# Kernel optimization log

Measured on AMD Instinct MI355X. Metric: run time of the kernel, lower is better.

The kernel has to match this reference:

```python
import jax, jax.numpy as jnp
import numpy as np

D = 128          # fine voxel grid resolution
N0 = 250000
D_IN, D_BASE, D_OUT = 16, 8, 8
EPS = 1e-5
# (cin, cout) for conv0..conv6, conv7, conv9, conv11
_CH = [(16, 8), (8, 16), (16, 16), (16, 32), (32, 32), (32, 64), (64, 64), (64, 32), (32, 16), (16, 8)]

def _offsets():
    r = np.arange(-1, 2)
    return np.stack(np.meshgrid(r, r, r, indexing='ij'), -1).reshape(-1, 3)  # [27,3]

def _lookup_fn(coords, d):
    keys = (coords[:, 0].astype(np.int64) * d + coords[:, 1]) * d + coords[:, 2]
    order = np.argsort(keys)
    skeys = keys[order]
    def lookup(q):
        valid = ((q >= 0) & (q < d)).all(-1)
        k = (q[:, 0].astype(np.int64) * d + q[:, 1]) * d + q[:, 2]
        pos = np.clip(np.searchsorted(skeys, k), 0, len(skeys) - 1)
        return np.where(valid & (skeys[pos] == k), order[pos], -1).astype(np.int32)
    return lookup

def _nbr_same(coords, d):
    # stride-1 sparse conv: outputs at input coords, neighbors at coord+k
    lk = _lookup_fn(coords, d)
    return np.stack([lk(coords + o) for o in _offsets()], 1)  # [N,27]

def _nbr_down(c_out, c_in, d_in):
    # stride-2 conv: output p gathers inputs at 2p+k
    lk = _lookup_fn(c_in, d_in)
    return np.stack([lk(c_out * 2 + o) for o in _offsets()], 1)

def _nbr_up(c_out, c_in, d_in):
    # transposed stride-2 conv: output q gathers input p=(q-k)/2 where divisible
    lk = _lookup_fn(c_in, d_in)
    cols = []
    for o in _offsets():
        q = c_out - o
        div = (q % 2 == 0).all(-1)
        cols.append(np.where(div, lk(q // 2), -1).astype(np.int32))
    return np.stack(cols, 1)

def setup_inputs():
    rng = np.random.default_rng(0)
    flat = rng.choice(D ** 3, size=N0, replace=False)
    c0 = np.stack([flat // (D * D), (flat // D) % D, flat % D], 1).astype(np.int32)
    c1 = np.unique(c0 // 2, axis=0)
    c2 = np.unique(c1 // 2, axis=0)
    c3 = np.unique(c2 // 2, axis=0)
    inp = {
        'feats': jax.random.normal(jax.random.key(0), (N0, D_IN), jnp.float32),
        'nbr0': jnp.asarray(_nbr_same(c0, D)),
        'nbr_d01': jnp.asarray(_nbr_down(c1, c0, D)),
        'nbr1': jnp.asarray(_nbr_same(c1, D // 2)),
        'nbr_d12': jnp.asarray(_nbr_down(c2, c1, D // 2)),
        'nbr2': jnp.asarray(_nbr_same(c2, D // 4)),
        'nbr_d23': jnp.asarray(_nbr_down(c3, c2, D // 4)),
        'nbr3': jnp.asarray(_nbr_same(c3, D // 8)),
        'nbr_u32': jnp.asarray(_nbr_up(c2, c3, D // 8)),
        'nbr_u21': jnp.asarray(_nbr_up(c1, c2, D // 4)),
        'nbr_u10': jnp.asarray(_nbr_up(c0, c1, D // 2)),
    }
    key = jax.random.key(1)
    for i, (ci, co) in enumerate(_CH):
        key, kw = jax.random.split(key)
        inp['w%d' % i] = jax.random.normal(kw, (27, ci, co), jnp.float32) / np.sqrt(27.0 * ci)
        inp['g%d' % i] = jnp.ones((co,), jnp.float32)
        inp['b%d' % i] = jnp.zeros((co,), jnp.float32)
    inp['lin_w'] = jax.random.normal(jax.random.key(2), (D_OUT, D_BASE), jnp.float32) / np.sqrt(D_BASE)
    return inp

def _sconv_bn_relu(f, nbr, w, g, b):
    # f: [Nin,Cin], nbr: [Nout,27] (-1 = no neighbor), w: [27,Cin,Cout]
    gth = jnp.where((nbr >= 0)[..., None], f[jnp.maximum(nbr, 0)], 0.0)  # [Nout,27,Cin]
    y = jnp.einsum('nkc,kco->no', gth, w)
    mu = y.mean(0)                       # training-mode BatchNorm over active voxels
    var = y.var(0)
    return jax.nn.relu((y - mu) * jax.lax.rsqrt(var + EPS) * g + b)

def reference(feats, nbr0, nbr_d01, nbr1, nbr_d12, nbr2, nbr_d23, nbr3, nbr_u32, nbr_u21, nbr_u10,
              w0, g0, b0, w1, g1, b1, w2, g2, b2, w3, g3, b3, w4, g4, b4,
              w5, g5, b5, w6, g6, b6, w7, g7, b7, w8, g8, b8, w9, g9, b9, lin_w):
    c0f = _sconv_bn_relu(feats, nbr0, w0, g0, b0)
    c2f = _sconv_bn_relu(_sconv_bn_relu(c0f, nbr_d01, w1, g1, b1), nbr1, w2, g2, b2)
    c4f = _sconv_bn_relu(_sconv_bn_relu(c2f, nbr_d12, w3, g3, b3), nbr2, w4, g4, b4)
    x = _sconv_bn_relu(_sconv_bn_relu(c4f, nbr_d23, w5, g5, b5), nbr3, w6, g6, b6)
    x = c4f + _sconv_bn_relu(x, nbr_u32, w7, g7, b7)
    x = c2f + _sconv_bn_relu(x, nbr_u21, w8, g8, b8)
    x = c0f + _sconv_bn_relu(x, nbr_u10, w9, g9, b9)
    return x @ lin_w.T, x
```

## Files before the change

kernel.cpp:

```cpp
#include <hip/hip_runtime.h>

#define EPSV 1e-5f
#define NBUCKET 64

typedef __attribute__((ext_vector_type(8))) short short8;
typedef __attribute__((ext_vector_type(4))) float float4v;

static inline int cdiv(int a, int b) { return (a + b - 1) / b; }
static inline int imin(int a, int b) { return a < b ? a : b; }

__device__ inline unsigned short f2bf(float x) {
  unsigned u = __float_as_uint(x);
  return (unsigned short)((u + 0x7FFFu + ((u >> 16) & 1u)) >> 16);
}
__device__ inline float bf2f(unsigned short u) {
  return __uint_as_float(((unsigned)u) << 16);
}

struct PrepArgs {
  const float* w[10];
  unsigned short* wt[10];
  int ci[10];
  int co[10];
  int wcum[11];
  const float* feats;
  unsigned short* featsb;
  int nfeat4;
  float* stats;
};

__global__ __launch_bounds__(256) void prep_kernel(PrepArgs p, long total) {
  const int nstat4 = 10 * NBUCKET * 128 / 4;
  for (long tid0 = (long)blockIdx.x * 256 + threadIdx.x; tid0 < total;
       tid0 += (long)gridDim.x * 256) {
    long tid = tid0;
    if (tid < nstat4) {
      ((float4*)p.stats)[tid] = make_float4(0.f, 0.f, 0.f, 0.f);
      continue;
    }
    tid -= nstat4;
    if (tid < p.nfeat4) {
      float4 v = ((const float4*)p.feats)[tid];
      ushort4 r;
      r.x = f2bf(v.x); r.y = f2bf(v.y); r.z = f2bf(v.z); r.w = f2bf(v.w);
      ((ushort4*)p.featsb)[tid] = r;
      continue;
    }
    tid -= p.nfeat4;
    if (tid >= p.wcum[10]) continue;
    int i = 0;
    while (tid >= p.wcum[i + 1]) ++i;
    int e = (int)(tid - p.wcum[i]);
    int ci = p.ci[i], co = p.co[i];
    int k = e / (ci * co);
    int r = e - k * (ci * co);
    int o = r / ci;
    int c = r - o * ci;
    p.wt[i][((long)k * co + o) * ci + c] = f2bf(p.w[i][((long)k * ci + c) * co + o]);
  }
}

template<int CI, int CO, int MINW>
__global__ __launch_bounds__(256, MINW) void conv_mfma(
    const unsigned short* __restrict__ f, const int* __restrict__ nbr,
    const unsigned short* __restrict__ wt, unsigned short* __restrict__ y,
    float* __restrict__ stats, int nout, int ntiles) {
  constexpr int NCHUNK = (CI == 8) ? 7 : (CI == 16) ? 14 : (CI == 32) ? 27 : 54;
  constexpr int CIP = (CI == 64) ? 64 : (CI == 32) ? 40 : 24;

  __shared__ int nbrT[64 * 27];
  __shared__ unsigned short Bs[27 * 16 * CIP];

  const int tid = threadIdx.x;
  const int lane = tid & 63;
  const int wid = tid >> 6;
  const int m = lane & 15;
  const int quad = lane >> 4;
  const int cbase = blockIdx.y * 16;
  const int co = cbase + m;
  const bool cok = co < CO;

  auto tapof = [&](int c) -> int {
    if constexpr (CI == 8) return c * 4 + quad;
    else if constexpr (CI == 16) return c * 2 + (quad >> 1);
    else if constexpr (CI == 32) return c;
    else return c >> 1;
  };
  auto cioof = [&](int c) -> int {
    if constexpr (CI == 8) return 0;
    else if constexpr (CI == 16) return (quad & 1) * 8;
    else if constexpr (CI == 32) return quad * 8;
    else return ((c & 1) << 5) + quad * 8;
  };
  auto baddr = [&](int tap, int mm, int cio) -> int {
    if constexpr (CI == 64) {
      int byt = (tap * 16 + mm) * 128 + cio * 2;
      byt ^= (mm & 7) << 4;
      return byt >> 1;
    } else {
      return (tap * 16 + mm) * CIP + cio;
    }
  };

  {
    constexpr int NC8 = CI / 8;
    for (int t = tid; t < 27 * 16 * NC8; t += 256) {
      int tap = t / (16 * NC8);
      int r = t - tap * (16 * NC8);
      int mo = r / NC8;
      int c8 = (r - mo * NC8) * 8;
      short8 v;
#pragma unroll
      for (int q = 0; q < 8; ++q) v[q] = 0;
      int c = cbase + mo;
      if (c < CO) v = *(const short8*)(wt + ((long)tap * CO + c) * CI + c8);
      *(short8*)&Bs[baddr(tap, mo, c8)] = v;
    }
  }

  const int nb8 = (int)gridDim.x >> 3;
  const int xcd = (int)blockIdx.x & 7;
  const int slot = (int)blockIdx.x >> 3;
  const int tq8 = ntiles >> 3, tr8 = ntiles & 7;
  const int t0 = xcd * tq8 + (xcd < tr8 ? xcd : tr8);
  const int tcnt = tq8 + (xcd < tr8 ? 1 : 0);

  float sum = 0.f, sq = 0.f;

  for (int ti = slot; ti < tcnt; ti += nb8) {
    const int tile = t0 + ti;
    const int rowb0 = tile * 64;
    {
      const long base = (long)rowb0 * 27;
      const long lim = (long)nout * 27;
      for (int j = tid; j < 432; j += 256) {
        long g = base + j * 4;
        int4 v;
        if (g + 4 <= lim) {
          v = *(const int4*)(nbr + g);
        } else {
          v.x = (g + 0 < lim) ? nbr[g + 0] : -1;
          v.y = (g + 1 < lim) ? nbr[g + 1] : -1;
          v.z = (g + 2 < lim) ? nbr[g + 2] : -1;
          v.w = (g + 3 < lim) ? nbr[g + 3] : -1;
        }
        *(int4*)&nbrT[j * 4] = v;
      }
    }
    __syncthreads();

    const int rowb = rowb0 + wid * 16;
    const int lrow = (wid * 16 + m) * 27;
    float4v acc = {0.f, 0.f, 0.f, 0.f};

    if constexpr (CI <= 16) {
      int idxs[NCHUNK];
#pragma unroll
      for (int c = 0; c < NCHUNK; ++c) {
        int tap = tapof(c);
        idxs[c] = (tap < 27) ? nbrT[lrow + tap] : -1;
      }
      short8 A[NCHUNK];
#pragma unroll
      for (int c = 0; c < NCHUNK; ++c) {
        short8 a;
#pragma unroll
        for (int q = 0; q < 8; ++q) a[q] = 0;
        if (idxs[c] >= 0) a = *(const short8*)(f + (long)idxs[c] * CI + cioof(c));
        A[c] = a;
      }
#pragma unroll
      for (int c = 0; c < NCHUNK; ++c) {
        int tap = tapof(c);
        int tapc = tap < 27 ? tap : 26;
        short8 bf = *(const short8*)&Bs[baddr(tapc, m, cioof(c))];
        acc = __builtin_amdgcn_mfma_f32_16x16x32_bf16(A[c], bf, acc, 0, 0, 0);
      }
    } else {
      constexpr int G = 9;
      constexpr int NG = NCHUNK / G;
      short8 A[2][G];
      auto load_group = [&](int g, int bi) {
#pragma unroll
        for (int j = 0; j < G; ++j) {
          const int c = g * G + j;
          const int tap = tapof(c);
          int idx = nbrT[lrow + tap];
          short8 a;
#pragma unroll
          for (int q = 0; q < 8; ++q) a[q] = 0;
          if (idx >= 0) a = *(const short8*)(f + (long)idx * CI + cioof(c));
          A[bi][j] = a;
        }
      };
      load_group(0, 0);
#pragma unroll
      for (int g = 0; g < NG; ++g) {
        const int cur = g & 1;
        if (g + 1 < NG) load_group(g + 1, cur ^ 1);
#pragma unroll
        for (int j = 0; j < G; ++j) {
          const int c = g * G + j;
          short8 bf = *(const short8*)&Bs[baddr(tapof(c), m, cioof(c))];
          acc = __builtin_amdgcn_mfma_f32_16x16x32_bf16(A[cur][j], bf, acc, 0, 0, 0);
        }
      }
    }

#pragma unroll
    for (int r = 0; r < 4; ++r) {
      float v = acc[r];
      int orow = rowb + quad * 4 + r;
      if (cok && orow < nout) y[(long)orow * CO + co] = f2bf(v);
      sum += v;
      sq = fmaf(v, v, sq);
    }
    __syncthreads();
  }

  sum += __shfl_xor(sum, 16); sq += __shfl_xor(sq, 16);
  sum += __shfl_xor(sum, 32); sq += __shfl_xor(sq, 32);
  if (quad == 0 && cok) {
    float* st = stats + ((((unsigned)blockIdx.x * 4 + wid) & (NBUCKET - 1)) << 7);
    atomicAdd(&st[co], sum);
    atomicAdd(&st[64 + co], sq);
  }
}

template<int CO>
__global__ __launch_bounds__(256) void bn_relu_bf16(
    const unsigned short* __restrict__ y, const float* __restrict__ stats,
    const float* __restrict__ g, const float* __restrict__ b,
    const unsigned short* __restrict__ skip, unsigned short* __restrict__ out,
    int nout, float inv_n) {
  __shared__ float sA[CO], sC[CO];
  if ((int)threadIdx.x < CO) {
    int o = threadIdx.x;
    float su = 0.f, sq = 0.f;
#pragma unroll 8
    for (int bk = 0; bk < NBUCKET; ++bk) {
      su += stats[bk * 128 + o];
      sq += stats[bk * 128 + 64 + o];
    }
    float mu = su * inv_n;
    float var = sq * inv_n - mu * mu;
    float a = g[o] * rsqrtf(var + EPSV);
    sA[o] = a;
    sC[o] = fmaf(-mu, a, b[o]);
  }
  __syncthreads();
  long total4 = (long)nout * CO / 4;
  for (long i4 = (long)blockIdx.x * 256 + threadIdx.x; i4 < total4;
       i4 += (long)gridDim.x * 256) {
    int o = (int)((i4 * 4) % CO);
    ushort4 v = ((const ushort4*)y)[i4];
    float vv[4] = {bf2f(v.x), bf2f(v.y), bf2f(v.z), bf2f(v.w)};
    unsigned short rr[4];
#pragma unroll
    for (int j = 0; j < 4; ++j) {
      float x = fmaxf(fmaf(vv[j], sA[o + j], sC[o + j]), 0.f);
      if (skip) x += bf2f(skip[i4 * 4 + j]);
      rr[j] = f2bf(x);
    }
    ushort4 r;
    r.x = rr[0]; r.y = rr[1]; r.z = rr[2]; r.w = rr[3];
    ((ushort4*)out)[i4] = r;
  }
}

__global__ __launch_bounds__(256) void tail_kernel(
    const unsigned short* __restrict__ c0f, const float* __restrict__ st9,
    const float* __restrict__ g9, const float* __restrict__ b9, float inv_n,
    const float* __restrict__ lin_w, const unsigned short* __restrict__ y9,
    float* __restrict__ out0, float* __restrict__ x0, int n0) {
  __shared__ float swl[64];
  __shared__ float sbn[16];
  if (threadIdx.x < 64) swl[threadIdx.x] = lin_w[threadIdx.x];
  if (threadIdx.x < 8) {
    int o = threadIdx.x;
    float su = 0.f, sq = 0.f;
#pragma unroll 8
    for (int bk = 0; bk < NBUCKET; ++bk) {
      su += st9[bk * 128 + o];
      sq += st9[bk * 128 + 64 + o];
    }
    float mu = su * inv_n;
    float var = sq * inv_n - mu * mu;
    float a = g9[o] * rsqrtf(var + EPSV);
    sbn[o] = a;
    sbn[8 + o] = fmaf(-mu, a, b9[o]);
  }
  __syncthreads();
  for (int n = blockIdx.x * 256 + (int)threadIdx.x; n < n0; n += gridDim.x * 256) {
    const ushort4* pr = (const ushort4*)(y9 + (long)n * 8);
    ushort4 r0 = pr[0], r1 = pr[1];
    unsigned short rw[8] = {r0.x, r0.y, r0.z, r0.w, r1.x, r1.y, r1.z, r1.w};
    const ushort4* pc = (const ushort4*)(c0f + (long)n * 8);
    ushort4 c0 = pc[0], c1 = pc[1];
    unsigned short cs[8] = {c0.x, c0.y, c0.z, c0.w, c1.x, c1.y, c1.z, c1.w};
    float xv[8];
#pragma unroll
    for (int c = 0; c < 8; ++c)
      xv[c] = bf2f(cs[c]) + fmaxf(fmaf(bf2f(rw[c]), sbn[c], sbn[8 + c]), 0.f);
    *(float4*)(x0 + (long)n * 8) = make_float4(xv[0], xv[1], xv[2], xv[3]);
    *(float4*)(x0 + (long)n * 8 + 4) = make_float4(xv[4], xv[5], xv[6], xv[7]);
    float ov[8];
#pragma unroll
    for (int j = 0; j < 8; ++j) {
      float s = 0.f;
#pragma unroll
      for (int c = 0; c < 8; ++c) s = fmaf(xv[c], swl[j * 8 + c], s);
      ov[j] = s;
    }
    *(float4*)(out0 + (long)n * 8) = make_float4(ov[0], ov[1], ov[2], ov[3]);
    *(float4*)(out0 + (long)n * 8 + 4) = make_float4(ov[4], ov[5], ov[6], ov[7]);
  }
}

extern "C" void kernel_launch(void* const* d_in, const int* in_sizes, int n_in,
                              void* d_out, int out_size, void* d_ws, size_t ws_size,
                              hipStream_t stream) {
  const float* feats   = (const float*)d_in[0];
  const int* nbr0      = (const int*)d_in[1];
  const int* nbr_d01   = (const int*)d_in[2];
  const int* nbr1      = (const int*)d_in[3];
  const int* nbr_d12   = (const int*)d_in[4];
  const int* nbr2      = (const int*)d_in[5];
  const int* nbr_d23   = (const int*)d_in[6];
  const int* nbr3      = (const int*)d_in[7];
  const int* nbr_u32   = (const int*)d_in[8];
  const int* nbr_u21   = (const int*)d_in[9];
  const int* nbr_u10   = (const int*)d_in[10];
  const float* w[10];
  const float* g[10];
  const float* b[10];
  for (int i = 0; i < 10; ++i) {
    w[i] = (const float*)d_in[11 + 3 * i];
    g[i] = (const float*)d_in[12 + 3 * i];
    b[i] = (const float*)d_in[13 + 3 * i];
  }
  const float* lin_w = (const float*)d_in[41];

  const int N0 = in_sizes[0] / 16;
  const int N1 = in_sizes[2] / 27;
  const int N2 = in_sizes[4] / 27;
  const int N3 = in_sizes[6] / 27;
  const float i0 = 1.f / N0, i1 = 1.f / N1, i2 = 1.f / N2, i3 = 1.f / N3;

  static const int CIv[10] = {16, 8, 16, 16, 32, 32, 64, 64, 32, 16};
  static const int COv[10] = {8, 16, 16, 32, 32, 64, 64, 32, 16, 8};

  float* stats = (float*)d_ws;
  unsigned short* u = (unsigned short*)(stats + 10 * NBUCKET * 128);

  unsigned short* yraw = u; u += (size_t)N1 * 32;

  unsigned short* wt[10];
  int wcum[11];
  wcum[0] = 0;
  for (int i = 0; i < 10; ++i) {
    wt[i] = u;
    int sz = 27 * CIv[i] * COv[i];
    u += sz;
    wcum[i + 1] = wcum[i] + sz;
  }
  unsigned short* featsb = u; u += (size_t)N0 * 16;
  unsigned short* c0f = u;    u += (size_t)N0 * 8;
  unsigned short* t1  = u;    u += (size_t)N1 * 16;
  unsigned short* c2f = u;    u += (size_t)N1 * 16;
  unsigned short* t2  = u;    u += (size_t)N2 * 32;
  unsigned short* c4f = u;    u += (size_t)N2 * 32;
  unsigned short* t3  = u;    u += (size_t)N3 * 64;
  unsigned short* t4  = u;    u += (size_t)N3 * 64;
  unsigned short* t5  = t2;
  unsigned short* t6  = t1;
  float* out0 = (float*)d_out;
  float* x0   = (float*)d_out + (size_t)N0 * 8;

  float* s[10];
  for (int i = 0; i < 10; ++i) s[i] = stats + i * NBUCKET * 128;

  PrepArgs pa;
  for (int i = 0; i < 10; ++i) {
    pa.w[i] = w[i]; pa.wt[i] = wt[i];
    pa.ci[i] = CIv[i]; pa.co[i] = COv[i];
    pa.wcum[i] = wcum[i];
  }
  pa.wcum[10] = wcum[10];
  pa.feats = feats; pa.featsb = featsb;
  pa.nfeat4 = N0 * 16 / 4;
  pa.stats = stats;
  long prep_total = (10 * NBUCKET * 128 / 4) + pa.nfeat4 + wcum[10];
  prep_kernel<<<imin((int)((prep_total + 255) / 256), 2048), 256, 0, stream>>>(pa, prep_total);

  auto bgrid = [](long nout, int co) {
    return imin((int)((nout * co / 4 + 255) / 256), 1024);
  };
  auto cgrid = [](int ntiles) {
    int g = (ntiles + 7) & ~7;
    if (g < 8) g = 8;
    return imin(g, 2048);
  };

  int tb0 = cdiv(N0, 64), tb1 = cdiv(N1, 64), tb2 = cdiv(N2, 64), tb3 = cdiv(N3, 64);

  conv_mfma<16, 8, 4><<<dim3(cgrid(tb0), 1), 256, 0, stream>>>(featsb, nbr0, wt[0], yraw, s[0], N0, tb0);
  bn_relu_bf16<8><<<bgrid(N0, 8), 256, 0, stream>>>(yraw, s[0], g[0], b[0], nullptr, c0f, N0, i0);

  conv_mfma<8, 16, 4><<<dim3(cgrid(tb1), 1), 256, 0, stream>>>(c0f, nbr_d01, wt[1], yraw, s[1], N1, tb1);
  bn_relu_bf16<16><<<bgrid(N1, 16), 256, 0, stream>>>(yraw, s[1], g[1], b[1], nullptr, t1, N1, i1);

  conv_mfma<16, 16, 4><<<dim3(cgrid(tb1), 1), 256, 0, stream>>>(t1, nbr1, wt[2], yraw, s[2], N1, tb1);
  bn_relu_bf16<16><<<bgrid(N1, 16), 256, 0, stream>>>(yraw, s[2], g[2], b[2], nullptr, c2f, N1, i1);

  conv_mfma<16, 32, 4><<<dim3(cgrid(tb2), 2), 256, 0, stream>>>(c2f, nbr_d12, wt[3], yraw, s[3], N2, tb2);
  bn_relu_bf16<32><<<bgrid(N2, 32), 256, 0, stream>>>(yraw, s[3], g[3], b[3], nullptr, t2, N2, i2);

  conv_mfma<32, 32, 3><<<dim3(cgrid(tb2), 2), 256, 0, stream>>>(t2, nbr2, wt[4], yraw, s[4], N2, tb2);
  bn_relu_bf16<32><<<bgrid(N2, 32), 256, 0, stream>>>(yraw, s[4], g[4], b[4], nullptr, c4f, N2, i2);

  conv_mfma<32, 64, 3><<<dim3(cgrid(tb3), 4), 256, 0, stream>>>(c4f, nbr_d23, wt[5], yraw, s[5], N3, tb3);
  bn_relu_bf16<64><<<bgrid(N3, 64), 256, 0, stream>>>(yraw, s[5], g[5], b[5], nullptr, t3, N3, i3);

  conv_mfma<64, 64, 2><<<dim3(cgrid(tb3), 4), 256, 0, stream>>>(t3, nbr3, wt[6], yraw, s[6], N3, tb3);
  bn_relu_bf16<64><<<bgrid(N3, 64), 256, 0, stream>>>(yraw, s[6], g[6], b[6], nullptr, t4, N3, i3);

  conv_mfma<64, 32, 2><<<dim3(cgrid(tb2), 2), 256, 0, stream>>>(t4, nbr_u32, wt[7], yraw, s[7], N2, tb2);
  bn_relu_bf16<32><<<bgrid(N2, 32), 256, 0, stream>>>(yraw, s[7], g[7], b[7], c4f, t5, N2, i2);

  conv_mfma<32, 16, 3><<<dim3(cgrid(tb1), 1), 256, 0, stream>>>(t5, nbr_u21, wt[8], yraw, s[8], N1, tb1);
  bn_relu_bf16<16><<<bgrid(N1, 16), 256, 0, stream>>>(yraw, s[8], g[8], b[8], c2f, t6, N1, i1);

  conv_mfma<16, 8, 4><<<dim3(cgrid(tb0), 1), 256, 0, stream>>>(t6, nbr_u10, wt[9], yraw, s[9], N0, tb0);

  tail_kernel<<<imin(cdiv(N0, 256), 1024), 256, 0, stream>>>(
      c0f, s[9], g[9], b[9], i0, lin_w, yraw, out0, x0, N0);
}
```

Baseline: 430.4 us.

## Launch one tile per conv block and shrink weight LDS for narrow outputs

```diff
diff --git a/kernel.cpp b/kernel.cpp
--- a/kernel.cpp
+++ b/kernel.cpp
@@ -64,17 +64,19 @@
 __global__ __launch_bounds__(256, MINW) void conv_mfma(
     const unsigned short* __restrict__ f, const int* __restrict__ nbr,
     const unsigned short* __restrict__ wt, unsigned short* __restrict__ y,
-    float* __restrict__ stats, int nout, int ntiles) {
+    float* __restrict__ stats, int nout) {
   constexpr int NCHUNK = (CI == 8) ? 7 : (CI == 16) ? 14 : (CI == 32) ? 27 : 54;
-  constexpr int CIP = (CI == 64) ? 64 : (CI == 32) ? 40 : 24;
+  constexpr int CIP = (CI == 64) ? 64 : (CI == 32) ? 40 : (CI == 16) ? 24 : 12;
+  constexpr int RB = (CO < 16) ? CO : 16;
 
   __shared__ int nbrT[64 * 27];
-  __shared__ unsigned short Bs[27 * 16 * CIP];
+  __shared__ unsigned short Bs[27 * RB * CIP];
 
   const int tid = threadIdx.x;
   const int lane = tid & 63;
   const int wid = tid >> 6;
   const int m = lane & 15;
+  const int mm = m & (RB - 1);
   const int quad = lane >> 4;
   const int cbase = blockIdx.y * 16;
   const int co = cbase + m;
@@ -92,21 +94,24 @@
     else if constexpr (CI == 32) return quad * 8;
     else return ((c & 1) << 5) + quad * 8;
   };
-  auto baddr = [&](int tap, int mm, int cio) -> int {
+  auto baddr = [&](int tap, int r, int cio) -> int {
     if constexpr (CI == 64) {
-      int byt = (tap * 16 + mm) * 128 + cio * 2;
-      byt ^= (mm & 7) << 4;
+      int byt = (tap * 16 + r) * 128 + cio * 2;
+      byt ^= (r & 7) << 4;
       return byt >> 1;
     } else {
-      return (tap * 16 + mm) * CIP + cio;
+      return (tap * RB + r) * CIP + cio;
     }
   };
+
+  const int tile = blockIdx.x;
+  const int rowb0 = tile * 64;
 
   {
     constexpr int NC8 = CI / 8;
-    for (int t = tid; t < 27 * 16 * NC8; t += 256) {
-      int tap = t / (16 * NC8);
-      int r = t - tap * (16 * NC8);
+    for (int t = tid; t < 27 * RB * NC8; t += 256) {
+      int tap = t / (RB * NC8);
+      int r = t - tap * (RB * NC8);
       int mo = r / NC8;
       int c8 = (r - mo * NC8) * 8;
       short8 v;
@@ -117,105 +122,91 @@
       *(short8*)&Bs[baddr(tap, mo, c8)] = v;
     }
   }
-
-  const int nb8 = (int)gridDim.x >> 3;
-  const int xcd = (int)blockIdx.x & 7;
-  const int slot = (int)blockIdx.x >> 3;
-  const int tq8 = ntiles >> 3, tr8 = ntiles & 7;
-  const int t0 = xcd * tq8 + (xcd < tr8 ? xcd : tr8);
-  const int tcnt = tq8 + (xcd < tr8 ? 1 : 0);
+  {
+    const long base = (long)rowb0 * 27;
+    const long lim = (long)nout * 27;
+    for (int j = tid; j < 432; j += 256) {
+      long g = base + j * 4;
+      int4 v;
+      if (g + 4 <= lim) {
+        v = *(const int4*)(nbr + g);
+      } else {
+        v.x = (g + 0 < lim) ? nbr[g + 0] : -1;
+        v.y = (g + 1 < lim) ? nbr[g + 1] : -1;
+        v.z = (g + 2 < lim) ? nbr[g + 2] : -1;
+        v.w = (g + 3 < lim) ? nbr[g + 3] : -1;
+      }
+      *(int4*)&nbrT[j * 4] = v;
+    }
+  }
+  __syncthreads();
+
+  const int rowb = rowb0 + wid * 16;
+  const int lrow = (wid * 16 + m) * 27;
+  float4v acc = {0.f, 0.f, 0.f, 0.f};
+
+  if constexpr (CI <= 16) {
+    int idxs[NCHUNK];
+#pragma unroll
+    for (int c = 0; c < NCHUNK; ++c) {
+      int tap = tapof(c);
+      idxs[c] = (tap < 27) ? nbrT[lrow + tap] : -1;
+    }
+    short8 A[NCHUNK];
+#pragma unroll
+    for (int c = 0; c < NCHUNK; ++c) {
+      short8 a;
+#pragma unroll
+      for (int q = 0; q < 8; ++q) a[q] = 0;
+      if (idxs[c] >= 0) a = *(const short8*)(f + (long)idxs[c] * CI + cioof(c));
+      A[c] = a;
+    }
+#pragma unroll
+    for (int c = 0; c < NCHUNK; ++c) {
+      int tap = tapof(c);
+      int tapc = tap < 27 ? tap : 26;
+      short8 bf = *(const short8*)&Bs[baddr(tapc, mm, cioof(c))];
+      acc = __builtin_amdgcn_mfma_f32_16x16x32_bf16(A[c], bf, acc, 0, 0, 0);
+    }
+  } else {
+    constexpr int G = 9;
+    constexpr int NG = NCHUNK / G;
+    short8 A[2][G];
+    auto load_group = [&](int g, int bi) {
+#pragma unroll
+      for (int j = 0; j < G; ++j) {
+        const int c = g * G + j;
+        const int tap = tapof(c);
+        int idx = nbrT[lrow + tap];
+        short8 a;
+#pragma unroll
+        for (int q = 0; q < 8; ++q) a[q] = 0;
+        if (idx >= 0) a = *(const short8*)(f + (long)idx * CI + cioof(c));
+        A[bi][j] = a;
+      }
+    };
+    load_group(0, 0);
+#pragma unroll
+    for (int g = 0; g < NG; ++g) {
+      const int cur = g & 1;
+      if (g + 1 < NG) load_group(g + 1, cur ^ 1);
+#pragma unroll
+      for (int j = 0; j < G; ++j) {
+        const int c = g * G + j;
+        short8 bf = *(const short8*)&Bs[baddr(tapof(c), mm, cioof(c))];
+        acc = __builtin_amdgcn_mfma_f32_16x16x32_bf16(A[cur][j], bf, acc, 0, 0, 0);
+      }
+    }
+  }
 
   float sum = 0.f, sq = 0.f;
-
-  for (int ti = slot; ti < tcnt; ti += nb8) {
-    const int tile = t0 + ti;
-    const int rowb0 = tile * 64;
-    {
-      const long base = (long)rowb0 * 27;
-      const long lim = (long)nout * 27;
-      for (int j = tid; j < 432; j += 256) {
-        long g = base + j * 4;
-        int4 v;
-        if (g + 4 <= lim) {
-          v = *(const int4*)(nbr + g);
-        } else {
-          v.x = (g + 0 < lim) ? nbr[g + 0] : -1;
-          v.y = (g + 1 < lim) ? nbr[g + 1] : -1;
-          v.z = (g + 2 < lim) ? nbr[g + 2] : -1;
-          v.w = (g + 3 < lim) ? nbr[g + 3] : -1;
-        }
-        *(int4*)&nbrT[j * 4] = v;
-      }
-    }
-    __syncthreads();
-
-    const int rowb = rowb0 + wid * 16;
-    const int lrow = (wid * 16 + m) * 27;
-    float4v acc = {0.f, 0.f, 0.f, 0.f};
-
-    if constexpr (CI <= 16) {
-      int idxs[NCHUNK];
-#pragma unroll
-      for (int c = 0; c < NCHUNK; ++c) {
-        int tap = tapof(c);
-        idxs[c] = (tap < 27) ? nbrT[lrow + tap] : -1;
-      }
-      short8 A[NCHUNK];
-#pragma unroll
-      for (int c = 0; c < NCHUNK; ++c) {
-        short8 a;
-#pragma unroll
-        for (int q = 0; q < 8; ++q) a[q] = 0;
-        if (idxs[c] >= 0) a = *(const short8*)(f + (long)idxs[c] * CI + cioof(c));
-        A[c] = a;
-      }
-#pragma unroll
-      for (int c = 0; c < NCHUNK; ++c) {
-        int tap = tapof(c);
-        int tapc = tap < 27 ? tap : 26;
-        short8 bf = *(const short8*)&Bs[baddr(tapc, m, cioof(c))];
-        acc = __builtin_amdgcn_mfma_f32_16x16x32_bf16(A[c], bf, acc, 0, 0, 0);
-      }
-    } else {
-      constexpr int G = 9;
-      constexpr int NG = NCHUNK / G;
-      short8 A[2][G];
-      auto load_group = [&](int g, int bi) {
-#pragma unroll
-        for (int j = 0; j < G; ++j) {
-          const int c = g * G + j;
-          const int tap = tapof(c);
-          int idx = nbrT[lrow + tap];
-          short8 a;
-#pragma unroll
-          for (int q = 0; q < 8; ++q) a[q] = 0;
-          if (idx >= 0) a = *(const short8*)(f + (long)idx * CI + cioof(c));
-          A[bi][j] = a;
-        }
-      };
-      load_group(0, 0);
-#pragma unroll
-      for (int g = 0; g < NG; ++g) {
-        const int cur = g & 1;
-        if (g + 1 < NG) load_group(g + 1, cur ^ 1);
-#pragma unroll
-        for (int j = 0; j < G; ++j) {
-          const int c = g * G + j;
-          short8 bf = *(const short8*)&Bs[baddr(tapof(c), m, cioof(c))];
-          acc = __builtin_amdgcn_mfma_f32_16x16x32_bf16(A[cur][j], bf, acc, 0, 0, 0);
-        }
-      }
-    }
-
-#pragma unroll
-    for (int r = 0; r < 4; ++r) {
-      float v = acc[r];
-      int orow = rowb + quad * 4 + r;
-      if (cok && orow < nout) y[(long)orow * CO + co] = f2bf(v);
-      sum += v;
-      sq = fmaf(v, v, sq);
-    }
-    __syncthreads();
+#pragma unroll
+  for (int r = 0; r < 4; ++r) {
+    float v = acc[r];
+    int orow = rowb + quad * 4 + r;
+    if (cok && orow < nout) y[(long)orow * CO + co] = f2bf(v);
+    sum += v;
+    sq = fmaf(v, v, sq);
   }
 
   sum += __shfl_xor(sum, 16); sq += __shfl_xor(sq, 16);
@@ -396,42 +387,37 @@
   auto bgrid = [](long nout, int co) {
     return imin((int)((nout * co / 4 + 255) / 256), 1024);
   };
-  auto cgrid = [](int ntiles) {
-    int g = (ntiles + 7) & ~7;
-    if (g < 8) g = 8;
-    return imin(g, 2048);
-  };
 
   int tb0 = cdiv(N0, 64), tb1 = cdiv(N1, 64), tb2 = cdiv(N2, 64), tb3 = cdiv(N3, 64);
 
-  conv_mfma<16, 8, 4><<<dim3(cgrid(tb0), 1), 256, 0, stream>>>(featsb, nbr0, wt[0], yraw, s[0], N0, tb0);
+  conv_mfma<16, 8, 6><<<dim3(tb0, 1), 256, 0, stream>>>(featsb, nbr0, wt[0], yraw, s[0], N0);
   bn_relu_bf16<8><<<bgrid(N0, 8), 256, 0, stream>>>(yraw, s[0], g[0], b[0], nullptr, c0f, N0, i0);
 
-  conv_mfma<8, 16, 4><<<dim3(cgrid(tb1), 1), 256, 0, stream>>>(c0f, nbr_d01, wt[1], yraw, s[1], N1, tb1);
+  conv_mfma<8, 16, 6><<<dim3(tb1, 1), 256, 0, stream>>>(c0f, nbr_d01, wt[1], yraw, s[1], N1);
   bn_relu_bf16<16><<<bgrid(N1, 16), 256, 0, stream>>>(yraw, s[1], g[1], b[1], nullptr, t1, N1, i1);
 
-  conv_mfma<16, 16, 4><<<dim3(cgrid(tb1), 1), 256, 0, stream>>>(t1, nbr1, wt[2], yraw, s[2], N1, tb1);
+  conv_mfma<16, 16, 5><<<dim3(tb1, 1), 256, 0, stream>>>(t1, nbr1, wt[2], yraw, s[2], N1);
   bn_relu_bf16<16><<<bgrid(N1, 16), 256, 0, stream>>>(yraw, s[2], g[2], b[2], nullptr, c2f, N1, i1);
 
-  conv_mfma<16, 32, 4><<<dim3(cgrid(tb2), 2), 256, 0, stream>>>(c2f, nbr_d12, wt[3], yraw, s[3], N2, tb2);
+  conv_mfma<16, 32, 5><<<dim3(tb2, 2), 256, 0, stream>>>(c2f, nbr_d12, wt[3], yraw, s[3], N2);
   bn_relu_bf16<32><<<bgrid(N2, 32), 256, 0, stream>>>(yraw, s[3], g[3], b[3], nullptr, t2, N2, i2);
 
-  conv_mfma<32, 32, 3><<<dim3(cgrid(tb2), 2), 256, 0, stream>>>(t2, nbr2, wt[4], yraw, s[4], N2, tb2);
+  conv_mfma<32, 32, 3><<<dim3(tb2, 2), 256, 0, stream>>>(t2, nbr2, wt[4], yraw, s[4], N2);
   bn_relu_bf16<32><<<bgrid(N2, 32), 256, 0, stream>>>(yraw, s[4], g[4], b[4], nullptr, c4f, N2, i2);
 
-  conv_mfma<32, 64, 3><<<dim3(cgrid(tb3), 4), 256, 0, stream>>>(c4f, nbr_d23, wt[5], yraw, s[5], N3, tb3);
+  conv_mfma<32, 64, 3><<<dim3(tb3, 4), 256, 0, stream>>>(c4f, nbr_d23, wt[5], yraw, s[5], N3);
   bn_relu_bf16<64><<<bgrid(N3, 64), 256, 0, stream>>>(yraw, s[5], g[5], b[5], nullptr, t3, N3, i3);
 
-  conv_mfma<64, 64, 2><<<dim3(cgrid(tb3), 4), 256, 0, stream>>>(t3, nbr3, wt[6], yraw, s[6], N3, tb3);
+  conv_mfma<64, 64, 2><<<dim3(tb3, 4), 256, 0, stream>>>(t3, nbr3, wt[6], yraw, s[6], N3);
   bn_relu_bf16<64><<<bgrid(N3, 64), 256, 0, stream>>>(yraw, s[6], g[6], b[6], nullptr, t4, N3, i3);
 
-  conv_mfma<64, 32, 2><<<dim3(cgrid(tb2), 2), 256, 0, stream>>>(t4, nbr_u32, wt[7], yraw, s[7], N2, tb2);
+  conv_mfma<64, 32, 2><<<dim3(tb2, 2), 256, 0, stream>>>(t4, nbr_u32, wt[7], yraw, s[7], N2);
   bn_relu_bf16<32><<<bgrid(N2, 32), 256, 0, stream>>>(yraw, s[7], g[7], b[7], c4f, t5, N2, i2);
 
-  conv_mfma<32, 16, 3><<<dim3(cgrid(tb1), 1), 256, 0, stream>>>(t5, nbr_u21, wt[8], yraw, s[8], N1, tb1);
+  conv_mfma<32, 16, 3><<<dim3(tb1, 1), 256, 0, stream>>>(t5, nbr_u21, wt[8], yraw, s[8], N1);
   bn_relu_bf16<16><<<bgrid(N1, 16), 256, 0, stream>>>(yraw, s[8], g[8], b[8], c2f, t6, N1, i1);
 
-  conv_mfma<16, 8, 4><<<dim3(cgrid(tb0), 1), 256, 0, stream>>>(t6, nbr_u10, wt[9], yraw, s[9], N0, tb0);
+  conv_mfma<16, 8, 6><<<dim3(tb0, 1), 256, 0, stream>>>(t6, nbr_u10, wt[9], yraw, s[9], N0);
 
   tail_kernel<<<imin(cdiv(N0, 256), 1024), 256, 0, stream>>>(
       c0f, s[9], g[9], b[9], i0, lin_w, yraw, out0, x0, N0);
```

New measurement: 428.2 us. No clear change (-0.5%).
